# Kernel tuning notes

Measured on AMD Instinct MI355X. Metric: run time of the kernel, lower is better.

The kernel has to match this reference:

```python
import jax, jax.numpy as jnp
import numpy as np

K = 5
K2 = K * K  # 25
SLOPE = 0.01  # torch leaky_relu default


def _unfold(x, k):
    # torch.nn.Unfold(k) on reflect-padded x: channel order c-major, then kh, kw
    b, c, h, w = x.shape
    p = k // 2
    xp = jnp.pad(x, ((0, 0), (0, 0), (p, p), (p, p)), mode='reflect')
    cols = jnp.stack([xp[:, :, i:i + h, j:j + w] for i in range(k) for j in range(k)], axis=2)
    return cols.reshape(b, c * k * k, h * w)  # (b, 3*k^2, h*w)


def _lin(x, W, b):
    # torch Linear: W is (out, in)
    return x @ W.T + b


def _lrelu(x):
    return jnp.where(x >= 0, x, SLOPE * x)


def setup_inputs() -> dict:
    key = jax.random.key(0)
    ks = iter(jax.random.split(key, 64))
    d = {}
    d['x'] = jax.random.uniform(next(ks), (4, 3, 384, 384), dtype=jnp.float32)

    def mk(name, out_f, in_f):
        d['W_' + name] = jax.random.normal(next(ks), (out_f, in_f), jnp.float32) * (1.0 / np.sqrt(in_f))
        d['b_' + name] = jax.random.normal(next(ks), (out_f,), jnp.float32) * 0.01

    mk('input', 2 * K2, 3 * K2)
    mk('h1', 3 * K2, 2 * K2)
    mk('h2', 3 * K2, 3 * K2)
    mk('h3', 2 * K2, 2 * K2)
    mk('h4', 5 * K2, 2 * K2)
    mk('h5', 2 * K2, 5 * K2)
    mk('out', 3, 2 * K2)
    # encoder(3*k^2): in -> 3*in -> in -> 3
    mk('e1', 9 * K2, 3 * K2); mk('e2', 3 * K2, 9 * K2); mk('e3', 3, 3 * K2)
    # encoder(2*k^2)
    mk('f1', 6 * K2, 2 * K2); mk('f2', 2 * K2, 6 * K2); mk('f3', 3, 2 * K2)
    # decoder(2*k^2): 3 -> out -> 3*out -> out
    mk('d1', 2 * K2, 3); mk('d2', 6 * K2, 2 * K2); mk('d3', 2 * K2, 6 * K2)
    return d


def reference(x,
              W_input, b_input, W_h1, b_h1, W_h2, b_h2, W_h3, b_h3,
              W_h4, b_h4, W_h5, b_h5, W_out, b_out,
              W_e1, b_e1, W_e2, b_e2, W_e3, b_e3,
              W_f1, b_f1, W_f2, b_f2, W_f3, b_f3,
              W_d1, b_d1, W_d2, b_d2, W_d3, b_d3):
    b, c, h, w = x.shape
    sw = jnp.transpose(_unfold(x, K), (0, 2, 1))  # (b, h*w, 3*k^2)
    x1 = _lin(sw, W_input, b_input)
    x2 = _lrelu(_lin(x1, W_h1, b_h1))
    x3 = jnp.tanh(_lin(x2, W_h2, b_h2))
    x3_enc = _lin(_lin(_lin(x3, W_e1, b_e1), W_e2, b_e2), W_e3, b_e3)
    enc2_x1 = _lin(_lin(_lin(x1, W_f1, b_f1), W_f2, b_f2), W_f3, b_f3)
    x4 = _lrelu(x3_enc + enc2_x1)
    x4_dec = _lin(_lin(_lin(_lin(x4, W_d1, b_d1), W_d2, b_d2), W_d3, b_d3), W_h3, b_h3)
    x5 = jnp.tanh(_lin(x4_dec, W_h4, b_h4))
    x6 = _lin(x5, W_h5, b_h5) - x1
    x7 = _lrelu(_lin(x6, W_out, b_out))  # (b, h*w, 3)
    return jnp.transpose(x7, (0, 2, 1)).reshape(b, c, h, w)
```

## Files before the change

kernel.cpp:

```cpp
#include <hip/hip_runtime.h>


#define IW 384
#define HW (384 * 384)
#define NPIX (4 * HW)
#define MTILE 192
#define NBLK (NPIX / MTILE)

typedef _Float16 half8 __attribute__((ext_vector_type(8)));
typedef __fp16 fp16x2 __attribute__((ext_vector_type(2)));
typedef __attribute__((ext_vector_type(4))) float f32x4;
typedef __attribute__((ext_vector_type(4))) unsigned int uint4_;

#define MFMAH(A, B, C) __builtin_amdgcn_mfma_f32_16x16x32_f16((A), (B), (C), 0, 0, 0)

#define BA   0
#define B1   64
#define B2   144
#define BEF  224
#define BD   240
#define B4   304
#define B5   432
#define BOUT 496
#define BIAS_TOT 512

#define W_A0   0
#define W_A1   2048
#define W_A2   4096
#define W_H1A  6144
#define W_H1B  8704
#define W_H2A  11264
#define W_H2B  13824
#define W_H2C  16384
#define W_EF   18944
#define W_D    24064
#define W_H4C0 28160
#define W_H5C0 30208
#define W_OUT  44544
#define W_NI   45568
#define W_TOT  47616

#define STG_BE  24320
#define STG_BF  24336

__device__ __forceinline__ float lrelu(float v) { return fmaxf(v, 0.01f * v); }

#if __has_builtin(__builtin_amdgcn_exp2f)
#define EXP2F __builtin_amdgcn_exp2f
#else
#define EXP2F __builtin_exp2f
#endif

__device__ __forceinline__ float tanh_fast(float v) {
    float e = EXP2F(v * 2.8853900817779268f);
    return __builtin_fmaf(-2.0f, __builtin_amdgcn_rcpf(e + 1.0f), 1.0f);
}

__device__ __forceinline__ unsigned short f2h_bits(float v) {
    union { _Float16 h; unsigned short s; } u; u.h = (_Float16)v; return u.s;
}
__device__ __forceinline__ float h2f_bits(unsigned short s) {
    union { _Float16 h; unsigned short s; } u; u.s = s; return (float)u.h;
}
__device__ __forceinline__ unsigned packh2(float a, float b) {
    union { fp16x2 h; unsigned u; } u;
    u.h = __builtin_amdgcn_cvt_pkrtz(a, b);
    return u.u;
}

__device__ __forceinline__ void stage(float* dst, const float* __restrict__ src,
                                      int n, int tid) {
    int n4 = n >> 2;
    float4* d = (float4*)dst;
    const float4* s = (const float4*)src;
#pragma unroll 4
    for (int i = tid; i < n4; i += 256) d[i] = s[i];
    for (int i = (n4 << 2) + tid; i < n; i += 256) dst[i] = src[i];
}

__global__ __launch_bounds__(256) void setup_all(
    const float* __restrict__ W_input, const float* __restrict__ b_input,
    const float* __restrict__ W_h1,  const float* __restrict__ b_h1,
    const float* __restrict__ W_h2,  const float* __restrict__ b_h2,
    const float* __restrict__ W_h3,  const float* __restrict__ b_h3,
    const float* __restrict__ W_h4,  const float* __restrict__ b_h4,
    const float* __restrict__ W_h5,  const float* __restrict__ b_h5,
    const float* __restrict__ W_out, const float* __restrict__ b_out,
    const float* __restrict__ W_e1,  const float* __restrict__ b_e1,
    const float* __restrict__ W_e2,  const float* __restrict__ b_e2,
    const float* __restrict__ W_e3,  const float* __restrict__ b_e3,
    const float* __restrict__ W_f1,  const float* __restrict__ b_f1,
    const float* __restrict__ W_f2,  const float* __restrict__ b_f2,
    const float* __restrict__ W_f3,  const float* __restrict__ b_f3,
    const float* __restrict__ W_d1,  const float* __restrict__ b_d1,
    const float* __restrict__ W_d2,  const float* __restrict__ b_d2,
    const float* __restrict__ W_d3,  const float* __restrict__ b_d3,
    float* __restrict__ ws)
{
    const int tid = threadIdx.x;
    const int NT = 256;
    short* wimg = (short*)(ws + BIAS_TOT);

    if (blockIdx.x < 71) {
        const int soff[17] = {W_A0,W_A1,W_A2, W_H1A,W_H1B, W_H2A,W_H2B,W_H2C,
                              W_H4C0,W_H5C0, W_H4C0+4096,W_H5C0+4096,
                              W_H4C0+8192,W_H5C0+8192, W_H4C0+12288,W_H5C0+12288,
                              W_OUT};
        const int slay[17] = {0,0,0, 1,1, 2,2,2, 6,7, 6,7, 6,7, 6,7, 8};
        const int sNT[17]  = {4,4,4, 5,5, 5,5,5, 2,4, 2,4, 2,4, 2,4, 1};
        const int sKTS[17] = {1,1,1, 1,1, 1,1,1, 2,1, 2,1, 2,1, 2,1, 2};
        const int snb[17]  = {0,0,0, 0,0, 0,0,0, 0,0, 32,0, 64,0, 96,0, 0};
        const int skb[17]  = {0,32,64, 0,32, 0,32,64, 0,0, 0,32, 0,64, 0,96, 0};

        int seg = 0, local = blockIdx.x;
        while (seg < 16 && local >= sNT[seg] * sKTS[seg]) { local -= sNT[seg] * sKTS[seg]; seg++; }
        const int kts = sKTS[seg];
        const int kt = local % kts, nt = local / kts;
        const int lay = slay[seg];
        short* dst = wimg + soff[seg] + local * 512;

#pragma unroll
        for (int t = 0; t < 2; t++) {
            int idx = tid + t * 256;
            int j = idx & 7, lane = idx >> 3;
            int slot = (lay == 0) ? ((lane >> 4) * 8 + j)
                                  : (4 * (lane >> 4) + (j & 3) + 16 * (j >> 2));
            int n = snb[seg] + nt * 16 + (lane & 15);
            int k = skb[seg] + kt * 32 + slot;
            float v = 0.0f;
            switch (lay) {
                case 0: if (n < 50  && k < 75)  v = W_input[n * 75 + k]; break;
                case 1: if (n < 75  && k < 50)  v = W_h1[n * 50 + k]; break;
                case 2: if (n < 75  && k < 75)  v = W_h2[n * 75 + k]; break;
                case 6: if (n < 125 && k < 50)  v = W_h4[n * 50 + k]; break;
                case 7: if (n < 50  && k < 125) v = W_h5[n * 125 + k]; break;
                case 8: if (n < 3   && k < 50)  v = W_out[n * 50 + k]; break;
            }
            dst[idx] = (short)f2h_bits(v);
        }
        return;
    }

    if (blockIdx.x == 74) {
        for (int i = tid; i < BIAS_TOT; i += NT) {
            if (i >= BD && i < B4) continue;
            float v = 0.0f;
            if (i < B1)        { int o = i - BA;   if (o < 50)  v = b_input[o]; }
            else if (i < B2)   { int o = i - B1;   if (o < 75)  v = b_h1[o]; }
            else if (i < BEF)  { int o = i - B2;   if (o < 75)  v = b_h2[o]; }
            else if (i < BD)   { v = 0.0f; }
            else if (i < B5)   { int o = i - B4;   if (o < 125) v = b_h4[o]; }
            else if (i < BOUT) { int o = i - B5;   if (o < 50)  v = b_h5[o]; }
            else               { int o = i - BOUT; if (o < 3)   v = b_out[o]; }
            ws[i] = v;
        }
        for (int i = tid; i < 2048; i += NT) {
            int j = i & 7, lane = (i >> 3) & 63, nt = i >> 9;
            int n = nt * 16 + (lane & 15);
            int k = (nt >> 1) * 32 + 4 * (lane >> 4) + (j & 3) + 16 * (j >> 2);
            wimg[W_NI + i] = (short)f2h_bits(k == n ? -1.0f : 0.0f);
        }
        return;
    }

    __shared__ __align__(16) float A[17500];
    __shared__ float B[675];
    __shared__ float C[256];
    __shared__ float Dd[256];
    __shared__ float Es[256];
    __shared__ float S[232];

    if (blockIdx.x == 71) {
        stage(A, W_e2, 16875, tid);
        for (int i = tid; i < 225; i += NT) { Es[i] = W_e3[i]; C[i] = b_e1[i]; }
        __syncthreads();
        for (int o = tid; o < 675; o += NT) {
            int r = o / 225, c = o % 225;
            float s0 = 0.f, s1 = 0.f, s2 = 0.f;
#pragma unroll
            for (int t = 0; t < 75; t += 3) {
                s0 += Es[r * 75 + t]     * A[t * 225 + c];
                s1 += Es[r * 75 + t + 1] * A[(t + 1) * 225 + c];
                s2 += Es[r * 75 + t + 2] * A[(t + 2) * 225 + c];
            }
            B[o] = s0 + s1 + s2;
        }
        for (int o = tid; o < 75; o += NT) {
            float s0 = 0.f, s1 = 0.f, s2 = 0.f;
#pragma unroll
            for (int t = 0; t < 225; t += 3) {
                s0 += A[o * 225 + t]     * C[t];
                s1 += A[o * 225 + t + 1] * C[t + 1];
                s2 += A[o * 225 + t + 2] * C[t + 2];
            }
            Dd[o] = b_e2[o] + s0 + s1 + s2;
        }
        __syncthreads();
        stage(A, W_e1, 16875, tid);
        __syncthreads();
        for (int o = tid; o < 225; o += NT) {
            int r = o / 75, c = o % 75;
            float s0 = 0.f, s1 = 0.f, s2 = 0.f;
#pragma unroll
            for (int t = 0; t < 225; t += 3) {
                s0 += B[r * 225 + t]     * A[t * 75 + c];
                s1 += B[r * 225 + t + 1] * A[(t + 1) * 75 + c];
                s2 += B[r * 225 + t + 2] * A[(t + 2) * 75 + c];
            }
            S[o] = s0 + s1 + s2;
        }
        for (int o = tid; o < 16; o += NT) {
            float s = 0.0f;
            if (o < 3) {
                s = b_e3[o];
                for (int t = 0; t < 75; t++) s += Es[o * 75 + t] * Dd[t];
            }
            ws[STG_BE + o] = s;
        }
        __syncthreads();
        for (int i = tid; i < 3072; i += NT) {
            int j = i & 7, lane = (i >> 3) & 63, frag = i >> 9, pl = frag & 1, kt = frag >> 1;
            int n = lane & 15;
            int k = kt * 32 + 4 * (lane >> 4) + (j & 3) + 16 * (j >> 2);
            float v = (n < 3 && k < 75) ? S[n * 75 + k] : 0.0f;
            float hi = h2f_bits(f2h_bits(v));
            wimg[W_EF + i] = (short)(pl ? f2h_bits(v - hi) : f2h_bits(v));
        }
    } else if (blockIdx.x == 72) {
        stage(A,        W_f2, 7500, tid);
        stage(A + 7500, W_f1, 7500, tid);
        for (int i = tid; i < 150; i += NT) { Es[i] = W_f3[i]; C[i] = b_f1[i]; }
        __syncthreads();
        for (int o = tid; o < 450; o += NT) {
            int r = o / 150, c = o % 150;
            float s0 = 0.f, s1 = 0.f;
#pragma unroll
            for (int t = 0; t < 50; t += 2) {
                s0 += Es[r * 50 + t]     * A[t * 150 + c];
                s1 += Es[r * 50 + t + 1] * A[(t + 1) * 150 + c];
            }
            B[o] = s0 + s1;
        }
        for (int o = tid; o < 50; o += NT) {
            float s0 = 0.f, s1 = 0.f;
#pragma unroll
            for (int t = 0; t < 150; t += 2) {
                s0 += A[o * 150 + t]     * C[t];
                s1 += A[o * 150 + t + 1] * C[t + 1];
            }
            Dd[o] = b_f2[o] + s0 + s1;
        }
        __syncthreads();
        for (int o = tid; o < 150; o += NT) {
            int r = o / 50, c = o % 50;
            float s0 = 0.f, s1 = 0.f;
#pragma unroll
            for (int t = 0; t < 150; t += 2) {
                s0 += B[r * 150 + t]     * A[7500 + t * 50 + c];
                s1 += B[r * 150 + t + 1] * A[7500 + (t + 1) * 50 + c];
            }
            S[o] = s0 + s1;
        }
        for (int o = tid; o < 16; o += NT) {
            float s = 0.0f;
            if (o < 3) {
                s = b_f3[o];
                for (int t = 0; t < 50; t++) s += Es[o * 50 + t] * Dd[t];
            }
            ws[STG_BF + o] = s;
        }
        __syncthreads();
        for (int i = tid; i < 2048; i += NT) {
            int j = i & 7, lane = (i >> 3) & 63, frag = i >> 9, pl = frag & 1, kt = frag >> 1;
            int n = lane & 15;
            int k = kt * 32 + 4 * (lane >> 4) + (j & 3) + 16 * (j >> 2);
            float v = (n < 3 && k < 50) ? S[n * 50 + k] : 0.0f;
            float hi = h2f_bits(f2h_bits(v));
            wimg[W_EF + 3072 + i] = (short)(pl ? f2h_bits(v - hi) : f2h_bits(v));
        }
    } else {
        stage(A,         W_d2, 7500, tid);
        stage(A + 7500,  W_d3, 7500, tid);
        stage(A + 15000, W_h3, 2500, tid);
        for (int i = tid; i < 150; i += NT) Es[i] = W_d1[i];
        for (int i = tid; i < 50;  i += NT) C[i] = b_d1[i];
        __syncthreads();
        for (int o = tid; o < 450; o += NT) {
            int r = o / 3, c = o % 3;
            float s0 = 0.f, s1 = 0.f;
#pragma unroll
            for (int t = 0; t < 50; t += 2) {
                s0 += A[r * 50 + t]     * Es[t * 3 + c];
                s1 += A[r * 50 + t + 1] * Es[(t + 1) * 3 + c];
            }
            B[o] = s0 + s1;
        }
        for (int o = tid; o < 150; o += NT) {
            float s0 = 0.f, s1 = 0.f;
#pragma unroll
            for (int t = 0; t < 50; t += 2) {
                s0 += A[o * 50 + t]     * C[t];
                s1 += A[o * 50 + t + 1] * C[t + 1];
            }
            Dd[o] = b_d2[o] + s0 + s1;
        }
        __syncthreads();
        for (int o = tid; o < 150; o += NT) {
            int r = o / 3, c = o % 3;
            float s0 = 0.f, s1 = 0.f;
#pragma unroll
            for (int t = 0; t < 150; t += 2) {
                s0 += A[7500 + r * 150 + t]     * B[t * 3 + c];
                s1 += A[7500 + r * 150 + t + 1] * B[(t + 1) * 3 + c];
            }
            Es[o] = s0 + s1;
        }
        for (int o = tid; o < 50; o += NT) {
            float s0 = 0.f, s1 = 0.f;
#pragma unroll
            for (int t = 0; t < 150; t += 2) {
                s0 += A[7500 + o * 150 + t]     * Dd[t];
                s1 += A[7500 + o * 150 + t + 1] * Dd[t + 1];
            }
            C[o] = b_d3[o] + s0 + s1;
        }
        __syncthreads();
        for (int o = tid; o < 150; o += NT) {
            int r = o / 3, c = o % 3;
            float s0 = 0.f, s1 = 0.f;
#pragma unroll
            for (int t = 0; t < 50; t += 2) {
                s0 += A[15000 + r * 50 + t]     * Es[t * 3 + c];
                s1 += A[15000 + r * 50 + t + 1] * Es[(t + 1) * 3 + c];
            }
            S[o] = s0 + s1;
        }
        for (int o = tid; o < 64; o += NT) {
            float v = 0.0f;
            if (o < 50) {
                float s0 = 0.f, s1 = 0.f;
#pragma unroll
                for (int t = 0; t < 50; t += 2) {
                    s0 += A[15000 + o * 50 + t]     * C[t];
                    s1 += A[15000 + o * 50 + t + 1] * C[t + 1];
                }
                v = b_h3[o] + s0 + s1;
            }
            ws[BD + o] = v;
        }
        __syncthreads();
        for (int i = tid; i < 4096; i += NT) {
            int j = i & 7, lane = (i >> 3) & 63, frag = i >> 9, pl = frag & 1, nt = frag >> 1;
            int n = nt * 16 + (lane & 15);
            int k = 4 * (lane >> 4) + (j & 3) + 16 * (j >> 2);
            float v = (n < 50 && k < 3) ? S[n * 3 + k] : 0.0f;
            float hi = h2f_bits(f2h_bits(v));
            wimg[W_D + i] = (short)(pl ? f2h_bits(v - hi) : f2h_bits(v));
        }
    }
}

__device__ __forceinline__ half8 gfragH(const short* __restrict__ wl, int off) {
    return *(const half8*)(wl + off);
}

__device__ __forceinline__ half8 packB(f32x4 lo, f32x4 hi) {
    union { unsigned u32[4]; half8 v; } u;
    u.u32[0] = packh2(lo[0], lo[1]);
    u.u32[1] = packh2(lo[2], lo[3]);
    u.u32[2] = packh2(hi[0], hi[1]);
    u.u32[3] = packh2(hi[2], hi[3]);
    return u.v;
}
__device__ __forceinline__ half8 packB1(f32x4 lo) {
    union { unsigned u32[4]; half8 v; } u;
    u.u32[0] = packh2(lo[0], lo[1]);
    u.u32[1] = packh2(lo[2], lo[3]);
    u.u32[2] = 0u; u.u32[3] = 0u;
    return u.v;
}

__device__ __forceinline__ void st16(unsigned int* p, half8 v) {
    union { half8 h; uint4_ u; } c; c.h = v;
    *(uint4_*)p = c.u;
}
__device__ __forceinline__ half8 ld16(const unsigned int* p) {
    union { half8 h; uint4_ u; } c; c.u = *(const uint4_*)p;
    return c.h;
}

__device__ __forceinline__ f32x4 lrelu4(f32x4 v) {
    v[0] = lrelu(v[0]); v[1] = lrelu(v[1]); v[2] = lrelu(v[2]); v[3] = lrelu(v[3]);
    return v;
}
__device__ __forceinline__ f32x4 tanh4(f32x4 v) {
    v[0] = tanh_fast(v[0]); v[1] = tanh_fast(v[1]);
    v[2] = tanh_fast(v[2]); v[3] = tanh_fast(v[3]);
    return v;
}

__global__ __launch_bounds__(256, 4) void fused_mfma(
    const float* __restrict__ xin,
    const float* __restrict__ ws,
    float* __restrict__ out)
{
    __shared__ float patch[2940];
    __shared__ int stab[96];
    __shared__ unsigned int x1buf[6144];

    const int tid = threadIdx.x;
    const int wv = tid >> 6;
    const int lane = tid & 63;
    const int qd = lane >> 4;
    const int mcol = lane & 15;
    const short* __restrict__ wl = (const short*)(ws + BIAS_TOT) + lane * 8;

    const int g0 = blockIdx.x * MTILE;
    const int bb = g0 / HW;
    const int p0 = g0 - bb * HW;
    const int yb = p0 / IW;
    const int xblk = p0 - yb * IW;
    const float* __restrict__ xb = xin + bb * 3 * HW;

    unsigned int* xpark = x1buf + wv * 1536 + lane * 4;

    for (int e = tid; e < 2940; e += 256) {
        int cr = e / 196;
        int i  = e - cr * 196;
        int c  = cr / 5, r = cr - c * 5;
        int ty = yb + r - 2; ty = ty < 0 ? -ty : ty; ty = (766 - ty) < ty ? 766 - ty : ty;
        int tx = xblk - 2 + i; tx = tx < 0 ? -tx : tx; tx = (766 - tx) < tx ? 766 - tx : tx;
        patch[cr * 196 + i] = xb[c * HW + ty * IW + tx];
    }
    if (tid < 96) {
        int v = 0;
        if (tid < 75) {
            int c = tid / 25, rem = tid - 25 * c;
            int rr = rem / 5, ss = rem - 5 * rr;
            v = (c * 5 + rr) * 196 + ss;
        }
        stab[tid] = v;
    }
    __syncthreads();

    half8 swf[3][3];
    {
        int st[3][8];
#pragma unroll
        for (int kt = 0; kt < 3; kt++)
#pragma unroll
            for (int j = 0; j < 8; j++)
                st[kt][j] = stab[kt * 32 + qd * 8 + j];
#pragma unroll
        for (int pt = 0; pt < 3; pt++) {
            const int xloc = wv * 48 + pt * 16 + mcol;
#pragma unroll
            for (int kt = 0; kt < 3; kt++) {
                union { unsigned u32[4]; half8 v; } u;
#pragma unroll
                for (int jj = 0; jj < 8; jj += 2) {
                    float v0 = patch[st[kt][jj]     + xloc];
                    float v1 = patch[st[kt][jj + 1] + xloc];
                    if (kt == 2) {
                        int qq0 = 64 + qd * 8 + jj;
                        v0 = (qq0     < 75) ? v0 : 0.0f;
                        v1 = (qq0 + 1 < 75) ? v1 : 0.0f;
                    }
                    u.u32[jj >> 1] = packh2(v0, v1);
                }
                swf[kt][pt] = u.v;
            }
        }
    }

    f32x4 accA[4][3];
#pragma unroll
    for (int mt = 0; mt < 4; mt++) {
        f32x4 b = *(const f32x4*)(ws + BA + mt * 16 + qd * 4);
        accA[mt][0] = b; accA[mt][1] = b; accA[mt][2] = b;
    }
#pragma unroll
    for (int kt = 0; kt < 3; kt++)
#pragma unroll
        for (int mt = 0; mt < 4; mt++) {
            half8 w = gfragH(wl, W_A0 + kt * 2048 + mt * 512);
#pragma unroll
            for (int pt = 0; pt < 3; pt++)
                accA[mt][pt] = MFMAH(w, swf[kt][pt], accA[mt][pt]);
        }
    half8 x1f[2][3];
#pragma unroll
    for (int kt = 0; kt < 2; kt++)
#pragma unroll
        for (int pt = 0; pt < 3; pt++) {
            x1f[kt][pt] = packB(accA[2 * kt][pt], accA[2 * kt + 1][pt]);
            st16(xpark + kt * 768 + pt * 256, x1f[kt][pt]);
        }

    f32x4 acc1[5][3];
#pragma unroll
    for (int mt = 0; mt < 5; mt++) {
        f32x4 b = *(const f32x4*)(ws + B1 + mt * 16 + qd * 4);
        acc1[mt][0] = b; acc1[mt][1] = b; acc1[mt][2] = b;
    }
#pragma unroll
    for (int kt = 0; kt < 2; kt++)
#pragma unroll
        for (int mt = 0; mt < 5; mt++) {
            half8 w = gfragH(wl, W_H1A + kt * 2560 + mt * 512);
#pragma unroll
            for (int pt = 0; pt < 3; pt++)
                acc1[mt][pt] = MFMAH(w, x1f[kt][pt], acc1[mt][pt]);
        }
    half8 x2f[3][3];
#pragma unroll
    for (int pt = 0; pt < 3; pt++) {
        x2f[0][pt] = packB (lrelu4(acc1[0][pt]), lrelu4(acc1[1][pt]));
        x2f[1][pt] = packB (lrelu4(acc1[2][pt]), lrelu4(acc1[3][pt]));
        x2f[2][pt] = packB1(lrelu4(acc1[4][pt]));
    }

    f32x4 acc2[5][3];
#pragma unroll
    for (int mt = 0; mt < 5; mt++) {
        f32x4 b = *(const f32x4*)(ws + B2 + mt * 16 + qd * 4);
        acc2[mt][0] = b; acc2[mt][1] = b; acc2[mt][2] = b;
    }
#pragma unroll
    for (int kt = 0; kt < 3; kt++)
#pragma unroll
        for (int mt = 0; mt < 5; mt++) {
            half8 w = gfragH(wl, W_H2A + kt * 2560 + mt * 512);
#pragma unroll
            for (int pt = 0; pt < 3; pt++)
                acc2[mt][pt] = MFMAH(w, x2f[kt][pt], acc2[mt][pt]);
        }
    half8 x3f[3][3];
#pragma unroll
    for (int pt = 0; pt < 3; pt++) {
        x3f[0][pt] = packB (tanh4(acc2[0][pt]), tanh4(acc2[1][pt]));
        x3f[1][pt] = packB (tanh4(acc2[2][pt]), tanh4(acc2[3][pt]));
        x3f[2][pt] = packB1(tanh4(acc2[4][pt]));
    }
    half8 x1r[2][3];
#pragma unroll
    for (int kt = 0; kt < 2; kt++)
#pragma unroll
        for (int pt = 0; pt < 3; pt++)
            x1r[kt][pt] = ld16(xpark + kt * 768 + pt * 256);

    f32x4 accEF[3];
    {
        f32x4 be = *(const f32x4*)(ws + STG_BE + qd * 4);
        f32x4 bf = *(const f32x4*)(ws + STG_BF + qd * 4);
        f32x4 b = be + bf;
        accEF[0] = b; accEF[1] = b; accEF[2] = b;
    }
#pragma unroll
    for (int kt = 0; kt < 3; kt++) {
        half8 wh = gfragH(wl, W_EF + kt * 1024);
        half8 wo = gfragH(wl, W_EF + kt * 1024 + 512);
#pragma unroll
        for (int pt = 0; pt < 3; pt++) {
            accEF[pt] = MFMAH(wh, x3f[kt][pt], accEF[pt]);
            accEF[pt] = MFMAH(wo, x3f[kt][pt], accEF[pt]);
        }
    }
#pragma unroll
    for (int kt = 0; kt < 2; kt++) {
        half8 wh = gfragH(wl, W_EF + 3072 + kt * 1024);
        half8 wo = gfragH(wl, W_EF + 3072 + kt * 1024 + 512);
#pragma unroll
        for (int pt = 0; pt < 3; pt++) {
            accEF[pt] = MFMAH(wh, x1r[kt][pt], accEF[pt]);
            accEF[pt] = MFMAH(wo, x1r[kt][pt], accEF[pt]);
        }
    }
    half8 x4f[3];
#pragma unroll
    for (int pt = 0; pt < 3; pt++)
        x4f[pt] = packB1(lrelu4(accEF[pt]));

    f32x4 x6a[4][3];
#pragma unroll
    for (int mt = 0; mt < 4; mt++) {
        f32x4 b = *(const f32x4*)(ws + B5 + mt * 16 + qd * 4);
        half8 nI = gfragH(wl, W_NI + mt * 512);
#pragma unroll
        for (int pt = 0; pt < 3; pt++)
            x6a[mt][pt] = MFMAH(nI, x1r[mt >> 1][pt], b);
    }

#pragma unroll
    for (int h = 0; h < 2; h++) {
        f32x4 accD[2][3];
#pragma unroll
        for (int m2 = 0; m2 < 2; m2++) {
            f32x4 b = *(const f32x4*)(ws + BD + (h * 2 + m2) * 16 + qd * 4);
            accD[m2][0] = b; accD[m2][1] = b; accD[m2][2] = b;
        }
#pragma unroll
        for (int m2 = 0; m2 < 2; m2++) {
            int mt = h * 2 + m2;
            half8 wh = gfragH(wl, W_D + mt * 1024);
            half8 wo = gfragH(wl, W_D + mt * 1024 + 512);
#pragma unroll
            for (int pt = 0; pt < 3; pt++) {
                accD[m2][pt] = MFMAH(wh, x4f[pt], accD[m2][pt]);
                accD[m2][pt] = MFMAH(wo, x4f[pt], accD[m2][pt]);
            }
        }
#pragma unroll
        for (int pt = 0; pt < 3; pt++)
            st16(xpark + h * 768 + pt * 256, packB(accD[0][pt], accD[1][pt]));
    }

#pragma unroll
    for (int c = 0; c < 4; c++) {
        const unsigned int* xr = xpark;
        asm volatile("" : "+v"(xr));
        half8 xd[2][3];
#pragma unroll
        for (int kt = 0; kt < 2; kt++)
#pragma unroll
            for (int pt = 0; pt < 3; pt++)
                xd[kt][pt] = ld16(xr + kt * 768 + pt * 256);
        f32x4 acc5[2][3];
#pragma unroll
        for (int mt2 = 0; mt2 < 2; mt2++) {
            f32x4 b = *(const f32x4*)(ws + B4 + c * 32 + mt2 * 16 + qd * 4);
            acc5[mt2][0] = b; acc5[mt2][1] = b; acc5[mt2][2] = b;
        }
#pragma unroll
        for (int kt = 0; kt < 2; kt++)
#pragma unroll
            for (int mt2 = 0; mt2 < 2; mt2++) {
                half8 w = gfragH(wl, W_H4C0 + c * 4096 + (mt2 * 2 + kt) * 512);
#pragma unroll
                for (int pt = 0; pt < 3; pt++)
                    acc5[mt2][pt] = MFMAH(w, xd[kt][pt], acc5[mt2][pt]);
            }
        half8 chf[3];
#pragma unroll
        for (int pt = 0; pt < 3; pt++)
            chf[pt] = packB(tanh4(acc5[0][pt]), tanh4(acc5[1][pt]));
#pragma unroll
        for (int mt = 0; mt < 4; mt++) {
            half8 w = gfragH(wl, W_H5C0 + c * 4096 + mt * 512);
#pragma unroll
            for (int pt = 0; pt < 3; pt++)
                x6a[mt][pt] = MFMAH(w, chf[pt], x6a[mt][pt]);
        }
    }

    f32x4 accO[3];
    {
        f32x4 b = *(const f32x4*)(ws + BOUT + qd * 4);
        accO[0] = b; accO[1] = b; accO[2] = b;
    }
#pragma unroll
    for (int kt = 0; kt < 2; kt++) {
        half8 w = gfragH(wl, W_OUT + kt * 512);
#pragma unroll
        for (int pt = 0; pt < 3; pt++) {
            half8 x6f = packB(x6a[2 * kt][pt], x6a[2 * kt + 1][pt]);
            accO[pt] = MFMAH(w, x6f, accO[pt]);
        }
    }
    if (qd == 0) {
#pragma unroll
        for (int pt = 0; pt < 3; pt++) {
            int p = p0 + wv * 48 + pt * 16 + mcol;
#pragma unroll
            for (int r = 0; r < 3; r++)
                out[(bb * 3 + r) * HW + p] = lrelu(accO[pt][r]);
        }
    }
}

extern "C" void kernel_launch(void* const* d_in, const int* in_sizes, int n_in,
                              void* d_out, int out_size, void* d_ws, size_t ws_size,
                              hipStream_t stream)
{
    const float* xin = (const float*)d_in[0];
    float* ws = (float*)d_ws;

    setup_all<<<75, 256, 0, stream>>>(
        (const float*)d_in[1],  (const float*)d_in[2],
        (const float*)d_in[3],  (const float*)d_in[4],
        (const float*)d_in[5],  (const float*)d_in[6],
        (const float*)d_in[7],  (const float*)d_in[8],
        (const float*)d_in[9],  (const float*)d_in[10],
        (const float*)d_in[11], (const float*)d_in[12],
        (const float*)d_in[13], (const float*)d_in[14],
        (const float*)d_in[15], (const float*)d_in[16],
        (const float*)d_in[17], (const float*)d_in[18],
        (const float*)d_in[19], (const float*)d_in[20],
        (const float*)d_in[21], (const float*)d_in[22],
        (const float*)d_in[23], (const float*)d_in[24],
        (const float*)d_in[25], (const float*)d_in[26],
        (const float*)d_in[27], (const float*)d_in[28],
        (const float*)d_in[29], (const float*)d_in[30],
        (const float*)d_in[31], (const float*)d_in[32],
        ws);

    fused_mfma<<<NBLK, 256, 0, stream>>>(xin, ws, (float*)d_out);
}
```

Before: 241.4 us.

## Split layer GEMMs into output-row groups and fuse tanh into encoder MFMA

Restructures the input, h1 and h2 MFMA stages so each processes two 16-row output tiles at a time, using smaller accumulator arrays. An empty asm barrier on the weight pointer keeps the compiler from hoisting all fragment loads across groups. The h2 stage's tanh output is fed directly into the EF encoder MFMAs per group instead of materialising all x3 fragments. This aims to cut peak VGPR pressure and possibly raise occupancy, at the cost of less MFMA interleaving and scheduling freedom between groups.

```diff
diff --git a/kernel.cpp b/kernel.cpp
--- a/kernel.cpp
+++ b/kernel.cpp
@@ -473,81 +473,76 @@
         }
     }
 
-    f32x4 accA[4][3];
-#pragma unroll
-    for (int mt = 0; mt < 4; mt++) {
-        f32x4 b = *(const f32x4*)(ws + BA + mt * 16 + qd * 4);
-        accA[mt][0] = b; accA[mt][1] = b; accA[mt][2] = b;
-    }
-#pragma unroll
-    for (int kt = 0; kt < 3; kt++)
-#pragma unroll
-        for (int mt = 0; mt < 4; mt++) {
-            half8 w = gfragH(wl, W_A0 + kt * 2048 + mt * 512);
+    half8 x1f[2][3];
+#pragma unroll
+    for (int g = 0; g < 2; g++) {
+        const short* wlg = wl;
+        asm volatile("" : "+v"(wlg));
+        f32x4 acc[2][3];
+#pragma unroll
+        for (int m = 0; m < 2; m++) {
+            f32x4 b = *(const f32x4*)(ws + BA + (2 * g + m) * 16 + qd * 4);
+            acc[m][0] = b; acc[m][1] = b; acc[m][2] = b;
+        }
+#pragma unroll
+        for (int kt = 0; kt < 3; kt++)
+#pragma unroll
+            for (int m = 0; m < 2; m++) {
+                half8 w = gfragH(wlg, W_A0 + kt * 2048 + (2 * g + m) * 512);
+#pragma unroll
+                for (int pt = 0; pt < 3; pt++)
+                    acc[m][pt] = MFMAH(w, swf[kt][pt], acc[m][pt]);
+            }
+#pragma unroll
+        for (int pt = 0; pt < 3; pt++) {
+            x1f[g][pt] = packB(acc[0][pt], acc[1][pt]);
+            st16(xpark + g * 768 + pt * 256, x1f[g][pt]);
+        }
+    }
+
+    half8 x2f[3][3];
+#pragma unroll
+    for (int g = 0; g < 2; g++) {
+        const short* wlg = wl;
+        asm volatile("" : "+v"(wlg));
+        f32x4 acc[2][3];
+#pragma unroll
+        for (int m = 0; m < 2; m++) {
+            f32x4 b = *(const f32x4*)(ws + B1 + (2 * g + m) * 16 + qd * 4);
+            acc[m][0] = b; acc[m][1] = b; acc[m][2] = b;
+        }
+#pragma unroll
+        for (int kt = 0; kt < 2; kt++)
+#pragma unroll
+            for (int m = 0; m < 2; m++) {
+                half8 w = gfragH(wlg, W_H1A + kt * 2560 + (2 * g + m) * 512);
+#pragma unroll
+                for (int pt = 0; pt < 3; pt++)
+                    acc[m][pt] = MFMAH(w, x1f[kt][pt], acc[m][pt]);
+            }
+#pragma unroll
+        for (int pt = 0; pt < 3; pt++)
+            x2f[g][pt] = packB(lrelu4(acc[0][pt]), lrelu4(acc[1][pt]));
+    }
+    {
+        const short* wlg = wl;
+        asm volatile("" : "+v"(wlg));
+        f32x4 acc[3];
+        {
+            f32x4 b = *(const f32x4*)(ws + B1 + 4 * 16 + qd * 4);
+            acc[0] = b; acc[1] = b; acc[2] = b;
+        }
+#pragma unroll
+        for (int kt = 0; kt < 2; kt++) {
+            half8 w = gfragH(wlg, W_H1A + kt * 2560 + 4 * 512);
 #pragma unroll
             for (int pt = 0; pt < 3; pt++)
-                accA[mt][pt] = MFMAH(w, swf[kt][pt], accA[mt][pt]);
-        }
-    half8 x1f[2][3];
-#pragma unroll
-    for (int kt = 0; kt < 2; kt++)
-#pragma unroll
-        for (int pt = 0; pt < 3; pt++) {
-            x1f[kt][pt] = packB(accA[2 * kt][pt], accA[2 * kt + 1][pt]);
-            st16(xpark + kt * 768 + pt * 256, x1f[kt][pt]);
-        }
-
-    f32x4 acc1[5][3];
-#pragma unroll
-    for (int mt = 0; mt < 5; mt++) {
-        f32x4 b = *(const f32x4*)(ws + B1 + mt * 16 + qd * 4);
-        acc1[mt][0] = b; acc1[mt][1] = b; acc1[mt][2] = b;
-    }
-#pragma unroll
-    for (int kt = 0; kt < 2; kt++)
-#pragma unroll
-        for (int mt = 0; mt < 5; mt++) {
-            half8 w = gfragH(wl, W_H1A + kt * 2560 + mt * 512);
-#pragma unroll
-            for (int pt = 0; pt < 3; pt++)
-                acc1[mt][pt] = MFMAH(w, x1f[kt][pt], acc1[mt][pt]);
-        }
-    half8 x2f[3][3];
-#pragma unroll
-    for (int pt = 0; pt < 3; pt++) {
-        x2f[0][pt] = packB (lrelu4(acc1[0][pt]), lrelu4(acc1[1][pt]));
-        x2f[1][pt] = packB (lrelu4(acc1[2][pt]), lrelu4(acc1[3][pt]));
-        x2f[2][pt] = packB1(lrelu4(acc1[4][pt]));
-    }
-
-    f32x4 acc2[5][3];
-#pragma unroll
-    for (int mt = 0; mt < 5; mt++) {
-        f32x4 b = *(const f32x4*)(ws + B2 + mt * 16 + qd * 4);
-        acc2[mt][0] = b; acc2[mt][1] = b; acc2[mt][2] = b;
-    }
-#pragma unroll
-    for (int kt = 0; kt < 3; kt++)
-#pragma unroll
-        for (int mt = 0; mt < 5; mt++) {
-            half8 w = gfragH(wl, W_H2A + kt * 2560 + mt * 512);
-#pragma unroll
-            for (int pt = 0; pt < 3; pt++)
-                acc2[mt][pt] = MFMAH(w, x2f[kt][pt], acc2[mt][pt]);
-        }
-    half8 x3f[3][3];
-#pragma unroll
-    for (int pt = 0; pt < 3; pt++) {
-        x3f[0][pt] = packB (tanh4(acc2[0][pt]), tanh4(acc2[1][pt]));
-        x3f[1][pt] = packB (tanh4(acc2[2][pt]), tanh4(acc2[3][pt]));
-        x3f[2][pt] = packB1(tanh4(acc2[4][pt]));
-    }
-    half8 x1r[2][3];
-#pragma unroll
-    for (int kt = 0; kt < 2; kt++)
+                acc[pt] = MFMAH(w, x1f[kt][pt], acc[pt]);
+        }
 #pragma unroll
         for (int pt = 0; pt < 3; pt++)
-            x1r[kt][pt] = ld16(xpark + kt * 768 + pt * 256);
+            x2f[2][pt] = packB1(lrelu4(acc[pt]));
+    }
 
     f32x4 accEF[3];
     {
@@ -557,15 +552,63 @@
         accEF[0] = b; accEF[1] = b; accEF[2] = b;
     }
 #pragma unroll
-    for (int kt = 0; kt < 3; kt++) {
-        half8 wh = gfragH(wl, W_EF + kt * 1024);
-        half8 wo = gfragH(wl, W_EF + kt * 1024 + 512);
+    for (int g = 0; g < 2; g++) {
+        const short* wlg = wl;
+        asm volatile("" : "+v"(wlg));
+        f32x4 acc[2][3];
+#pragma unroll
+        for (int m = 0; m < 2; m++) {
+            f32x4 b = *(const f32x4*)(ws + B2 + (2 * g + m) * 16 + qd * 4);
+            acc[m][0] = b; acc[m][1] = b; acc[m][2] = b;
+        }
+#pragma unroll
+        for (int kt = 0; kt < 3; kt++)
+#pragma unroll
+            for (int m = 0; m < 2; m++) {
+                half8 w = gfragH(wlg, W_H2A + kt * 2560 + (2 * g + m) * 512);
+#pragma unroll
+                for (int pt = 0; pt < 3; pt++)
+                    acc[m][pt] = MFMAH(w, x2f[kt][pt], acc[m][pt]);
+            }
+        half8 wh = gfragH(wlg, W_EF + g * 1024);
+        half8 wo = gfragH(wlg, W_EF + g * 1024 + 512);
 #pragma unroll
         for (int pt = 0; pt < 3; pt++) {
-            accEF[pt] = MFMAH(wh, x3f[kt][pt], accEF[pt]);
-            accEF[pt] = MFMAH(wo, x3f[kt][pt], accEF[pt]);
-        }
-    }
+            half8 t = packB(tanh4(acc[0][pt]), tanh4(acc[1][pt]));
+            accEF[pt] = MFMAH(wh, t, accEF[pt]);
+            accEF[pt] = MFMAH(wo, t, accEF[pt]);
+        }
+    }
+    {
+        const short* wlg = wl;
+        asm volatile("" : "+v"(wlg));
+        f32x4 acc[3];
+        {
+            f32x4 b = *(const f32x4*)(ws + B2 + 4 * 16 + qd * 4);
+            acc[0] = b; acc[1] = b; acc[2] = b;
+        }
+#pragma unroll
+        for (int kt = 0; kt < 3; kt++) {
+            half8 w = gfragH(wlg, W_H2A + kt * 2560 + 4 * 512);
+#pragma unroll
+            for (int pt = 0; pt < 3; pt++)
+                acc[pt] = MFMAH(w, x2f[kt][pt], acc[pt]);
+        }
+        half8 wh = gfragH(wlg, W_EF + 2 * 1024);
+        half8 wo = gfragH(wlg, W_EF + 2 * 1024 + 512);
+#pragma unroll
+        for (int pt = 0; pt < 3; pt++) {
+            half8 t = packB1(tanh4(acc[pt]));
+            accEF[pt] = MFMAH(wh, t, accEF[pt]);
+            accEF[pt] = MFMAH(wo, t, accEF[pt]);
+        }
+    }
+    half8 x1r[2][3];
+#pragma unroll
+    for (int kt = 0; kt < 2; kt++)
+#pragma unroll
+        for (int pt = 0; pt < 3; pt++)
+            x1r[kt][pt] = ld16(xpark + kt * 768 + pt * 256);
 #pragma unroll
     for (int kt = 0; kt < 2; kt++) {
         half8 wh = gfragH(wl, W_EF + 3072 + kt * 1024);
```

Measured after the change: 217.2 us. 1.11x faster.
